# Optimization experiments

Hardware: AMD Instinct MI355X
Metric: run time of the kernel (lower is better)

## Reference

```python
import jax, jax.numpy as jnp
import numpy as np

N = 8192
IN_F = 512
OUT_F = 64
ALPHA = 0.2  # LeakyReLU negative slope
NEG_INF = -9e15


def setup_inputs() -> dict:
    key = jax.random.key(0)
    k1, k2, k3, k4 = jax.random.split(key, 4)
    inp = jax.random.normal(k1, (N, IN_F), dtype=jnp.float32)
    adj = jax.random.randint(k2, (N, N), 0, 2, dtype=jnp.int32)
    W = jax.random.normal(k3, (IN_F, OUT_F), dtype=jnp.float32) * (1.414 * (6.0 / (IN_F + OUT_F)) ** 0.5)
    a = jax.random.normal(k4, (2 * OUT_F, 1), dtype=jnp.float32) * (1.414 * (6.0 / (2 * OUT_F + 1)) ** 0.5)
    return {"input": inp, "adj": adj, "W": W, "a": a}


def reference(input, adj, W, a):
    h = input @ W                      # [N, F]
    F_ = h.shape[1]
    # e_ij = leakyrelu(a[:F].h_i + a[F:].h_j)  (equivalent to the concat form)
    f_src = h @ a[:F_, 0]              # [N]
    f_dst = h @ a[F_:, 0]              # [N]
    e = jax.nn.leaky_relu(f_src[:, None] + f_dst[None, :], negative_slope=ALPHA)  # [N, N]
    att = jnp.where(adj > 0, e, jnp.float32(NEG_INF))
    att = jax.nn.softmax(att, axis=1)  # dropout p is inert in eval mode
    h_prime = att @ h                  # [N, F]
    return jax.nn.elu(h_prime)         # concat=True
```

## Files before the change

kernel.cpp:

```cpp
#include <hip/hip_runtime.h>

#define N_NODES 8192
#define IN_F 512
#define OUT_F 64
#define LOG2E 1.4426950408889634f

typedef short bf16x8 __attribute__((ext_vector_type(8)));
typedef float f32x4 __attribute__((ext_vector_type(4)));

static __device__ __forceinline__ unsigned short f2bf(float f) {
  unsigned u = __float_as_uint(f);
  u = (u + 0x7fffu + ((u >> 16) & 1u)) >> 16;
  return (unsigned short)u;
}

__global__ __launch_bounds__(256) void k_gemm(const float* __restrict__ input,
                                              const float* __restrict__ W,
                                              const float* __restrict__ a,
                                              float* __restrict__ h,
                                              float* __restrict__ fsrcL,
                                              float* __restrict__ fdstL) {
  const int lane = threadIdx.x & 63;
  const int wv = threadIdx.x >> 6;
  const int row = blockIdx.x * 4 + wv;
  const float* inrow = input + (size_t)row * IN_F;
  const int c = lane;
  float acc = 0.f;
  for (int k = 0; k < IN_F; k += 4) {
    float4 x = *(const float4*)(inrow + k);
    acc += x.x * W[(k + 0) * OUT_F + c];
    acc += x.y * W[(k + 1) * OUT_F + c];
    acc += x.z * W[(k + 2) * OUT_F + c];
    acc += x.w * W[(k + 3) * OUT_F + c];
  }
  h[(size_t)row * OUT_F + c] = acc;
  float vs = acc * a[c];
  float vd = acc * a[OUT_F + c];
#pragma unroll
  for (int off = 32; off > 0; off >>= 1) {
    vs += __shfl_xor(vs, off, 64);
    vd += __shfl_xor(vd, off, 64);
  }
  if (lane == 0) {
    fsrcL[row] = vs * LOG2E;
    fdstL[row] = vd * LOG2E;
  }
}

__global__ __launch_bounds__(256) void k_max(const float* __restrict__ fdstL,
                                             float* __restrict__ ML) {
  float m = -3.0e38f;
  for (int i = threadIdx.x; i < N_NODES; i += 256) m = fmaxf(m, fdstL[i]);
#pragma unroll
  for (int off = 32; off > 0; off >>= 1) m = fmaxf(m, __shfl_xor(m, off, 64));
  __shared__ float sm[4];
  if ((threadIdx.x & 63) == 0) sm[threadIdx.x >> 6] = m;
  __syncthreads();
  if (threadIdx.x == 0) ML[0] = fmaxf(fmaxf(sm[0], sm[1]), fmaxf(sm[2], sm[3]));
}

__global__ __launch_bounds__(256) void k_transpose(const float* __restrict__ h,
                                                   unsigned short* __restrict__ hT) {
  __shared__ float t[64][65];
  const int r0 = blockIdx.x * 64;
#pragma unroll
  for (int q = 0; q < 16; q++) {
    int idx = q * 256 + threadIdx.x;
    int r = idx >> 6, c = idx & 63;
    t[c][r] = h[(size_t)(r0 + r) * OUT_F + c];
  }
  __syncthreads();
#pragma unroll
  for (int q = 0; q < 8; q++) {
    int idx = q * 256 + threadIdx.x;
    int c = idx >> 5, rp = idx & 31;
    float a0 = t[c][2 * rp], a1 = t[c][2 * rp + 1];
    unsigned pk = (unsigned)f2bf(a0) | ((unsigned)f2bf(a1) << 16);
    *(unsigned*)(hT + (size_t)c * N_NODES + r0 + 2 * rp) = pk;
  }
}

__global__ __launch_bounds__(256) void k_attn(const int* __restrict__ adj,
                                              const unsigned short* __restrict__ hT,
                                              const float* __restrict__ fsrcL,
                                              const float* __restrict__ fdstL,
                                              const float* __restrict__ MLp,
                                              float* __restrict__ out) {
  const int lane = threadIdx.x & 63;
  const int wv = threadIdx.x >> 6;
  const int i0 = blockIdx.x * 16;
  const int m = lane & 15;
  const int g = lane >> 4;

  const float MLv = MLp[0];
  const float fs = fsrcL[i0 + m];
  const float xm = fs + MLv;
  const float mL = fmaxf(xm, 0.2f * xm);

  f32x4 acc0{}, acc1{}, acc2{}, acc3{};
  float lpart = 0.f;

  const int* adjrow = adj + (size_t)(i0 + m) * N_NODES;
  const unsigned short* hT0 = hT + (size_t)m * N_NODES;

  const int jbeg = wv * (N_NODES / 4);
  const int jend = jbeg + (N_NODES / 4);
  for (int j0 = jbeg; j0 < jend; j0 += 64) {
#pragma unroll
    for (int s = 0; s < 2; s++) {
      const int jb = j0 + s * 32 + g * 8;
      int4 a0 = *(const int4*)(adjrow + jb);
      int4 a1 = *(const int4*)(adjrow + jb + 4);
      float4 d0 = *(const float4*)(fdstL + jb);
      float4 d1 = *(const float4*)(fdstL + jb + 4);
      bf16x8 b0 = *(const bf16x8*)(hT0 + jb);
      bf16x8 b1 = *(const bf16x8*)(hT0 + (size_t)16 * N_NODES + jb);
      bf16x8 b2 = *(const bf16x8*)(hT0 + (size_t)32 * N_NODES + jb);
      bf16x8 b3 = *(const bf16x8*)(hT0 + (size_t)48 * N_NODES + jb);

      int av[8] = {a0.x, a0.y, a0.z, a0.w, a1.x, a1.y, a1.z, a1.w};
      float dv[8] = {d0.x, d0.y, d0.z, d0.w, d1.x, d1.y, d1.z, d1.w};
      bf16x8 pa;
#pragma unroll
      for (int t = 0; t < 8; t++) {
        float x = fs + dv[t];
        float y = fmaxf(x, 0.2f * x) - mL;
        float p = __builtin_amdgcn_exp2f(y);
        p = av[t] ? p : 0.0f;
        lpart += p;
        pa[t] = (short)f2bf(p);
      }
      acc0 = __builtin_amdgcn_mfma_f32_16x16x32_bf16(pa, b0, acc0, 0, 0, 0);
      acc1 = __builtin_amdgcn_mfma_f32_16x16x32_bf16(pa, b1, acc1, 0, 0, 0);
      acc2 = __builtin_amdgcn_mfma_f32_16x16x32_bf16(pa, b2, acc2, 0, 0, 0);
      acc3 = __builtin_amdgcn_mfma_f32_16x16x32_bf16(pa, b3, acc3, 0, 0, 0);
    }
  }

  lpart += __shfl_xor(lpart, 16, 64);
  lpart += __shfl_xor(lpart, 32, 64);

  __shared__ float accbuf[4][16][64];
  __shared__ float lbuf[4][16];
#pragma unroll
  for (int r = 0; r < 4; r++) {
    accbuf[wv][g * 4 + r][0 + m]  = acc0[r];
    accbuf[wv][g * 4 + r][16 + m] = acc1[r];
    accbuf[wv][g * 4 + r][32 + m] = acc2[r];
    accbuf[wv][g * 4 + r][48 + m] = acc3[r];
  }
  if (lane < 16) lbuf[wv][lane] = lpart;
  __syncthreads();

#pragma unroll
  for (int q = 0; q < 4; q++) {
    int idx = q * 256 + threadIdx.x;
    int r = idx >> 6, c = idx & 63;
    float ssum = accbuf[0][r][c] + accbuf[1][r][c] + accbuf[2][r][c] + accbuf[3][r][c];
    float l = lbuf[0][r] + lbuf[1][r] + lbuf[2][r] + lbuf[3][r];
    float v = ssum / l;
    out[(size_t)(i0 + r) * OUT_F + c] =
        v > 0.f ? v : __builtin_amdgcn_exp2f(v * LOG2E) - 1.f;
  }
}

extern "C" void kernel_launch(void* const* d_in, const int* in_sizes, int n_in,
                              void* d_out, int out_size, void* d_ws, size_t ws_size,
                              hipStream_t stream) {
  const float* input = (const float*)d_in[0];
  const int* adj = (const int*)d_in[1];
  const float* W = (const float*)d_in[2];
  const float* a = (const float*)d_in[3];
  float* out = (float*)d_out;

  char* ws = (char*)d_ws;
  float* h = (float*)ws;
  unsigned short* hT = (unsigned short*)(ws + (2u << 20));
  float* fsrcL = (float*)(ws + (3u << 20));
  float* fdstL = (float*)(ws + (3u << 20) + 32 * 1024);
  float* ML = (float*)(ws + (3u << 20) + 64 * 1024);

  k_gemm<<<N_NODES / 4, 256, 0, stream>>>(input, W, a, h, fsrcL, fdstL);
  k_max<<<1, 256, 0, stream>>>(fdstL, ML);
  k_transpose<<<N_NODES / 64, 256, 0, stream>>>(h, hT);
  k_attn<<<N_NODES / 16, 256, 0, stream>>>(adj, hT, fsrcL, fdstL, ML, out);
}
```

Before: 480.2 us.

## Fuse transpose into GEMM, factor exp out of attention loop, use MFMA row sums

The GEMM kernel now writes bf16 transposed h directly, which removes the separate transpose kernel and the fp32 h buffer. The prep kernel precomputes exp2(fdst) and exp2(0.2*fdst) per column, so the inner attention loop swaps a per-element exp for a compare, a select and a multiply. Softmax row sums come from an extra MFMA against a ones vector instead of scalar accumulation. The attention kernel also moves to 512 threads, uses nontemporal adj loads and truncation-style bf16 packing via perm. The factorization could overflow or underflow for large fdst values, and it adds extra loads of E1 and E2.

Measured after the change: 516.4 us. 7.5% more time.

```diff
diff --git a/kernel.cpp b/kernel.cpp
--- a/kernel.cpp
+++ b/kernel.cpp
@@ -7,22 +7,18 @@
 
 typedef short bf16x8 __attribute__((ext_vector_type(8)));
 typedef float f32x4 __attribute__((ext_vector_type(4)));
-
-static __device__ __forceinline__ unsigned short f2bf(float f) {
-  unsigned u = __float_as_uint(f);
-  u = (u + 0x7fffu + ((u >> 16) & 1u)) >> 16;
-  return (unsigned short)u;
-}
+typedef int i32x4 __attribute__((ext_vector_type(4)));
 
 __global__ __launch_bounds__(256) void k_gemm(const float* __restrict__ input,
                                               const float* __restrict__ W,
                                               const float* __restrict__ a,
-                                              float* __restrict__ h,
+                                              unsigned short* __restrict__ hT,
                                               float* __restrict__ fsrcL,
                                               float* __restrict__ fdstL) {
   const int lane = threadIdx.x & 63;
   const int wv = threadIdx.x >> 6;
-  const int row = blockIdx.x * 4 + wv;
+  const int r0 = blockIdx.x * 4;
+  const int row = r0 + wv;
   const float* inrow = input + (size_t)row * IN_F;
   const int c = lane;
   float acc = 0.f;
@@ -33,7 +29,6 @@
     acc += x.z * W[(k + 2) * OUT_F + c];
     acc += x.w * W[(k + 3) * OUT_F + c];
   }
-  h[(size_t)row * OUT_F + c] = acc;
   float vs = acc * a[c];
   float vd = acc * a[OUT_F + c];
 #pragma unroll
@@ -45,12 +40,33 @@
     fsrcL[row] = vs * LOG2E;
     fdstL[row] = vd * LOG2E;
   }
+  __shared__ float hs[4][64];
+  hs[wv][c] = acc;
+  __syncthreads();
+  if (threadIdx.x < 64) {
+    const int cc = threadIdx.x;
+    unsigned u0 = __float_as_uint(hs[0][cc]) + 0x8000u;
+    unsigned u1 = __float_as_uint(hs[1][cc]) + 0x8000u;
+    unsigned u2 = __float_as_uint(hs[2][cc]) + 0x8000u;
+    unsigned u3 = __float_as_uint(hs[3][cc]) + 0x8000u;
+    uint2 pk;
+    pk.x = __builtin_amdgcn_perm(u1, u0, 0x07060302u);
+    pk.y = __builtin_amdgcn_perm(u3, u2, 0x07060302u);
+    *(uint2*)(hT + (size_t)cc * N_NODES + r0) = pk;
+  }
 }
 
-__global__ __launch_bounds__(256) void k_max(const float* __restrict__ fdstL,
-                                             float* __restrict__ ML) {
+__global__ __launch_bounds__(256) void k_prep(const float* __restrict__ fdstL,
+                                              float* __restrict__ ML,
+                                              float* __restrict__ E1,
+                                              float* __restrict__ E2) {
   float m = -3.0e38f;
-  for (int i = threadIdx.x; i < N_NODES; i += 256) m = fmaxf(m, fdstL[i]);
+  for (int i = threadIdx.x; i < N_NODES; i += 256) {
+    float v = fdstL[i];
+    E1[i] = __builtin_amdgcn_exp2f(v);
+    E2[i] = __builtin_amdgcn_exp2f(0.2f * v);
+    m = fmaxf(m, v);
+  }
 #pragma unroll
   for (int off = 32; off > 0; off >>= 1) m = fmaxf(m, __shfl_xor(m, off, 64));
   __shared__ float sm[4];
@@ -59,32 +75,12 @@
   if (threadIdx.x == 0) ML[0] = fmaxf(fmaxf(sm[0], sm[1]), fmaxf(sm[2], sm[3]));
 }
 
-__global__ __launch_bounds__(256) void k_transpose(const float* __restrict__ h,
-                                                   unsigned short* __restrict__ hT) {
-  __shared__ float t[64][65];
-  const int r0 = blockIdx.x * 64;
-#pragma unroll
-  for (int q = 0; q < 16; q++) {
-    int idx = q * 256 + threadIdx.x;
-    int r = idx >> 6, c = idx & 63;
-    t[c][r] = h[(size_t)(r0 + r) * OUT_F + c];
-  }
-  __syncthreads();
-#pragma unroll
-  for (int q = 0; q < 8; q++) {
-    int idx = q * 256 + threadIdx.x;
-    int c = idx >> 5, rp = idx & 31;
-    float a0 = t[c][2 * rp], a1 = t[c][2 * rp + 1];
-    unsigned pk = (unsigned)f2bf(a0) | ((unsigned)f2bf(a1) << 16);
-    *(unsigned*)(hT + (size_t)c * N_NODES + r0 + 2 * rp) = pk;
-  }
-}
-
-__global__ __launch_bounds__(256) void k_attn(const int* __restrict__ adj,
+__global__ __launch_bounds__(512) void k_attn(const int* __restrict__ adj,
                                               const unsigned short* __restrict__ hT,
                                               const float* __restrict__ fsrcL,
-                                              const float* __restrict__ fdstL,
                                               const float* __restrict__ MLp,
+                                              const float* __restrict__ E1,
+                                              const float* __restrict__ E2,
                                               float* __restrict__ out) {
   const int lane = threadIdx.x & 63;
   const int wv = threadIdx.x >> 6;
@@ -96,52 +92,59 @@
   const float fs = fsrcL[i0 + m];
   const float xm = fs + MLv;
   const float mL = fmaxf(xm, 0.2f * xm);
+  const float S1 = __builtin_amdgcn_exp2f(fs - mL);
+  const float S2 = __builtin_amdgcn_exp2f(0.2f * fs - mL);
+  const float Ti = __builtin_amdgcn_exp2f(-fs);
 
-  f32x4 acc0{}, acc1{}, acc2{}, acc3{};
-  float lpart = 0.f;
+  f32x4 acc0{}, acc1{}, acc2{}, acc3{}, acc4{};
+  union { unsigned w[4]; bf16x8 v; } ones;
+  ones.w[0] = ones.w[1] = ones.w[2] = ones.w[3] = 0x3F803F80u;
 
   const int* adjrow = adj + (size_t)(i0 + m) * N_NODES;
   const unsigned short* hT0 = hT + (size_t)m * N_NODES;
 
-  const int jbeg = wv * (N_NODES / 4);
-  const int jend = jbeg + (N_NODES / 4);
-  for (int j0 = jbeg; j0 < jend; j0 += 64) {
+  const int jbeg = wv * (N_NODES / 8);
+  for (int j0 = jbeg; j0 < jbeg + (N_NODES / 8); j0 += 64) {
 #pragma unroll
     for (int s = 0; s < 2; s++) {
       const int jb = j0 + s * 32 + g * 8;
-      int4 a0 = *(const int4*)(adjrow + jb);
-      int4 a1 = *(const int4*)(adjrow + jb + 4);
-      float4 d0 = *(const float4*)(fdstL + jb);
-      float4 d1 = *(const float4*)(fdstL + jb + 4);
+      i32x4 a0 = __builtin_nontemporal_load((const i32x4*)(adjrow + jb));
+      i32x4 a1 = __builtin_nontemporal_load((const i32x4*)(adjrow + jb) + 1);
+      float4 e1a = *(const float4*)(E1 + jb);
+      float4 e1b = *(const float4*)(E1 + jb + 4);
+      float4 e2a = *(const float4*)(E2 + jb);
+      float4 e2b = *(const float4*)(E2 + jb + 4);
       bf16x8 b0 = *(const bf16x8*)(hT0 + jb);
       bf16x8 b1 = *(const bf16x8*)(hT0 + (size_t)16 * N_NODES + jb);
       bf16x8 b2 = *(const bf16x8*)(hT0 + (size_t)32 * N_NODES + jb);
       bf16x8 b3 = *(const bf16x8*)(hT0 + (size_t)48 * N_NODES + jb);
 
-      int av[8] = {a0.x, a0.y, a0.z, a0.w, a1.x, a1.y, a1.z, a1.w};
-      float dv[8] = {d0.x, d0.y, d0.z, d0.w, d1.x, d1.y, d1.z, d1.w};
-      bf16x8 pa;
+      const int av[8] = {a0.x, a0.y, a0.z, a0.w, a1.x, a1.y, a1.z, a1.w};
+      const float e1v[8] = {e1a.x, e1a.y, e1a.z, e1a.w, e1b.x, e1b.y, e1b.z, e1b.w};
+      const float e2v[8] = {e2a.x, e2a.y, e2a.z, e2a.w, e2b.x, e2b.y, e2b.z, e2b.w};
+      unsigned u[8];
 #pragma unroll
       for (int t = 0; t < 8; t++) {
-        float x = fs + dv[t];
-        float y = fmaxf(x, 0.2f * x) - mL;
-        float p = __builtin_amdgcn_exp2f(y);
+        float p = (e1v[t] >= Ti) ? e1v[t] * S1 : e2v[t] * S2;
         p = av[t] ? p : 0.0f;
-        lpart += p;
-        pa[t] = (short)f2bf(p);
+        u[t] = __float_as_uint(p) + 0x8000u;
       }
-      acc0 = __builtin_amdgcn_mfma_f32_16x16x32_bf16(pa, b0, acc0, 0, 0, 0);
-      acc1 = __builtin_amdgcn_mfma_f32_16x16x32_bf16(pa, b1, acc1, 0, 0, 0);
-      acc2 = __builtin_amdgcn_mfma_f32_16x16x32_bf16(pa, b2, acc2, 0, 0, 0);
-      acc3 = __builtin_amdgcn_mfma_f32_16x16x32_bf16(pa, b3, acc3, 0, 0, 0);
+      union { unsigned w[4]; bf16x8 v; } pc;
+      pc.w[0] = __builtin_amdgcn_perm(u[1], u[0], 0x07060302u);
+      pc.w[1] = __builtin_amdgcn_perm(u[3], u[2], 0x07060302u);
+      pc.w[2] = __builtin_amdgcn_perm(u[5], u[4], 0x07060302u);
+      pc.w[3] = __builtin_amdgcn_perm(u[7], u[6], 0x07060302u);
+
+      acc0 = __builtin_amdgcn_mfma_f32_16x16x32_bf16(pc.v, b0, acc0, 0, 0, 0);
+      acc1 = __builtin_amdgcn_mfma_f32_16x16x32_bf16(pc.v, b1, acc1, 0, 0, 0);
+      acc2 = __builtin_amdgcn_mfma_f32_16x16x32_bf16(pc.v, b2, acc2, 0, 0, 0);
+      acc3 = __builtin_amdgcn_mfma_f32_16x16x32_bf16(pc.v, b3, acc3, 0, 0, 0);
+      acc4 = __builtin_amdgcn_mfma_f32_16x16x32_bf16(pc.v, ones.v, acc4, 0, 0, 0);
     }
   }
 
-  lpart += __shfl_xor(lpart, 16, 64);
-  lpart += __shfl_xor(lpart, 32, 64);
-
-  __shared__ float accbuf[4][16][64];
-  __shared__ float lbuf[4][16];
+  __shared__ float accbuf[8][16][64];
+  __shared__ float lbuf[8][16];
 #pragma unroll
   for (int r = 0; r < 4; r++) {
     accbuf[wv][g * 4 + r][0 + m]  = acc0[r];
@@ -149,15 +152,22 @@
     accbuf[wv][g * 4 + r][32 + m] = acc2[r];
     accbuf[wv][g * 4 + r][48 + m] = acc3[r];
   }
-  if (lane < 16) lbuf[wv][lane] = lpart;
+  if ((lane & 15) == 0) {
+#pragma unroll
+    for (int r = 0; r < 4; r++) lbuf[wv][g * 4 + r] = acc4[r];
+  }
   __syncthreads();
 
 #pragma unroll
-  for (int q = 0; q < 4; q++) {
-    int idx = q * 256 + threadIdx.x;
+  for (int q = 0; q < 2; q++) {
+    int idx = q * 512 + threadIdx.x;
     int r = idx >> 6, c = idx & 63;
-    float ssum = accbuf[0][r][c] + accbuf[1][r][c] + accbuf[2][r][c] + accbuf[3][r][c];
-    float l = lbuf[0][r] + lbuf[1][r] + lbuf[2][r] + lbuf[3][r];
+    float ssum = 0.f, l = 0.f;
+#pragma unroll
+    for (int w = 0; w < 8; w++) {
+      ssum += accbuf[w][r][c];
+      l += lbuf[w][r];
+    }
     float v = ssum / l;
     out[(size_t)(i0 + r) * OUT_F + c] =
         v > 0.f ? v : __builtin_amdgcn_exp2f(v * LOG2E) - 1.f;
@@ -174,14 +184,14 @@
   float* out = (float*)d_out;
 
   char* ws = (char*)d_ws;
-  float* h = (float*)ws;
-  unsigned short* hT = (unsigned short*)(ws + (2u << 20));
-  float* fsrcL = (float*)(ws + (3u << 20));
-  float* fdstL = (float*)(ws + (3u << 20) + 32 * 1024);
-  float* ML = (float*)(ws + (3u << 20) + 64 * 1024);
+  unsigned short* hT = (unsigned short*)ws;
+  float* fsrcL = (float*)(ws + (1u << 20));
+  float* fdstL = (float*)(ws + (1u << 20) + 32 * 1024);
+  float* ML = (float*)(ws + (1u << 20) + 64 * 1024);
+  float* E1 = (float*)(ws + (1u << 20) + 128 * 1024);
+  float* E2 = (float*)(ws + (1u << 20) + 160 * 1024);
 
-  k_gemm<<<N_NODES / 4, 256, 0, stream>>>(input, W, a, h, fsrcL, fdstL);
-  k_max<<<1, 256, 0, stream>>>(fdstL, ML);
-  k_transpose<<<N_NODES / 64, 256, 0, stream>>>(h, hT);
-  k_attn<<<N_NODES / 16, 256, 0, stream>>>(adj, hT, fsrcL, fdstL, ML, out);
+  k_gemm<<<N_NODES / 4, 256, 0, stream>>>(input, W, a, hT, fsrcL, fdstL);
+  k_prep<<<1, 256, 0, stream>>>(fdstL, ML, E1, E2);
+  k_attn<<<N_NODES / 16, 512, 0, stream>>>(adj, hT, fsrcL, ML, E1, E2, out);
 }
```
